# Kernel tuning notes

Hardware: AMD Instinct MI355X
Metric: run time of the kernel (lower is better)

Reference implementation:

```python
import jax, jax.numpy as jnp
import numpy as np

NUM_USERS = 100000
NUM_ITEMS = 50000
NUM_NODES = NUM_USERS + NUM_ITEMS
EMBED_DIM = 128
NUM_LAYERS = 3
CONTENT_DIM = 768
NUM_EDGES = 1000000
BATCH = 4096
LAMBDA_CONTENT = 0.1
INIT_STD = 0.1


def setup_inputs() -> dict:
    key = jax.random.key(0)
    ks = jax.random.split(key, 9)
    edge_index = jax.random.randint(ks[0], (2, NUM_EDGES), 0, NUM_NODES, dtype=jnp.int64 if jax.config.jax_enable_x64 else jnp.int32)
    edge_weight = jax.random.uniform(ks[1], (NUM_EDGES,), dtype=jnp.float32)
    batch_users = jax.random.randint(ks[2], (BATCH,), 0, NUM_USERS)
    batch_pos_items = jax.random.randint(ks[3], (BATCH,), 0, NUM_ITEMS)
    batch_neg_items = jax.random.randint(ks[4], (BATCH,), 0, NUM_ITEMS)
    item_content = jax.random.normal(ks[5], (NUM_ITEMS, CONTENT_DIM), dtype=jnp.float32)
    user_emb_w = INIT_STD * jax.random.normal(ks[6], (NUM_USERS, EMBED_DIM), dtype=jnp.float32)
    item_emb_w = INIT_STD * jax.random.normal(ks[7], (NUM_ITEMS, EMBED_DIM), dtype=jnp.float32)
    # nn.Linear(item_content_dim, embed_dim, bias=False): weight [embed_dim, content_dim]
    bound = 1.0 / np.sqrt(CONTENT_DIM)
    content_proj_w = jax.random.uniform(ks[8], (EMBED_DIM, CONTENT_DIM), minval=-bound, maxval=bound, dtype=jnp.float32)
    return {
        'edge_index': edge_index, 'edge_weight': edge_weight,
        'batch_users': batch_users, 'batch_pos_items': batch_pos_items,
        'batch_neg_items': batch_neg_items, 'item_content': item_content,
        'user_emb_w': user_emb_w, 'item_emb_w': item_emb_w,
        'content_proj_w': content_proj_w,
    }


def _lgconv(x, src, dst, ew, num_nodes):
    # PyG LGConv: gcn_norm(add_self_loops=False) then scatter-add at target.
    deg = jax.ops.segment_sum(ew, dst, num_segments=num_nodes)          # [N]
    dinv = jnp.where(deg > 0, jax.lax.rsqrt(deg), 0.0)
    norm = dinv[src] * ew * dinv[dst]                                    # [E]
    return jax.ops.segment_sum(norm[:, None] * x[src], dst, num_segments=num_nodes)


def _propagate(user_emb_w, item_emb_w, src, dst, ew):
    x = jnp.concatenate([user_emb_w, item_emb_w], axis=0)               # [N, D]
    acc = x
    for _ in range(NUM_LAYERS):
        x = _lgconv(x, src, dst, ew, NUM_NODES)
        acc = acc + x
    x_final = acc / (NUM_LAYERS + 1)
    return x_final[:NUM_USERS], x_final[NUM_USERS:]


def reference(edge_index, edge_weight, batch_users, batch_pos_items,
              batch_neg_items, item_content, user_emb_w, item_emb_w,
              content_proj_w):
    src, dst = edge_index[0], edge_index[1]
    u_final, i_final = _propagate(user_emb_w, item_emb_w, src, dst, edge_weight)
    u = u_final[batch_users]
    i_pos = i_final[batch_pos_items]
    i_neg = i_final[batch_neg_items]
    pos_score = jnp.sum(u * i_pos, axis=-1)
    neg_score = jnp.sum(u * i_neg, axis=-1)
    bpr = jnp.mean(jax.nn.softplus(-(pos_score - neg_score)))
    reg = jnp.mean(jnp.sum(u**2, axis=1) + jnp.sum(i_pos**2, axis=1) + jnp.sum(i_neg**2, axis=1)) * 1e-4
    proj = item_content @ content_proj_w.T                              # [I, D]
    align = jnp.mean((i_final - proj) ** 2)
    loss = bpr + reg + LAMBDA_CONTENT * align
    return loss, u_final, i_final
```

## Files before the change

kernel.cpp:

```cpp
#include <hip/hip_runtime.h>
#include <math.h>

#define NU 100000
#define NI 50000
#define NN 150000
#define D 128
#define NE 1000000
#define CD 768
#define BATCH 4096
#define NGEMM 782
#define NK (CD / 64)
#define PREPB 2832
#define ARMB 944

typedef short bf16x8 __attribute__((ext_vector_type(8)));
typedef float f32x4 __attribute__((ext_vector_type(4)));

static inline size_t alignup(size_t x, size_t a) { return (x + a - 1) / a * a; }

__device__ inline unsigned short f2bf(float f) {
  unsigned int u = __builtin_bit_cast(unsigned int, f);
  unsigned int r = (u + 0x7fffu + ((u >> 16) & 1u)) >> 16;
  return (unsigned short)r;
}
__device__ inline unsigned int pack2bf(float lo, float hi) {
  return (unsigned int)f2bf(lo) | ((unsigned int)f2bf(hi) << 16);
}
__device__ inline float bflo(unsigned int p) {
  return __builtin_bit_cast(float, p << 16);
}
__device__ inline float bfhi(unsigned int p) {
  return __builtin_bit_cast(float, p & 0xffff0000u);
}

#define ACC8(P, W)                                                        \
  a[0] = fmaf(W, bflo(P.x), a[0]); a[1] = fmaf(W, bfhi(P.x), a[1]);       \
  a[2] = fmaf(W, bflo(P.y), a[2]); a[3] = fmaf(W, bfhi(P.y), a[3]);       \
  a[4] = fmaf(W, bflo(P.z), a[4]); a[5] = fmaf(W, bfhi(P.z), a[5]);       \
  a[6] = fmaf(W, bflo(P.w), a[6]); a[7] = fmaf(W, bfhi(P.w), a[7]);

__device__ __forceinline__ void gather_rows(
    const int* __restrict__ row_ptr, const uint2* __restrict__ cedge,
    const uint4* __restrict__ xin, int n, int sub, float* a) {
  int beg = row_ptr[n], end = row_ptr[n + 1];
  int j = beg;
  for (; j + 4 <= end; j += 4) {
    uint2 e0 = cedge[j], e1 = cedge[j + 1], e2 = cedge[j + 2], e3 = cedge[j + 3];
    uint4 p0 = xin[(size_t)e0.x * 16 + sub];
    uint4 p1 = xin[(size_t)e1.x * 16 + sub];
    uint4 p2 = xin[(size_t)e2.x * 16 + sub];
    uint4 p3 = xin[(size_t)e3.x * 16 + sub];
    float w0 = __builtin_bit_cast(float, e0.y);
    float w1 = __builtin_bit_cast(float, e1.y);
    float w2 = __builtin_bit_cast(float, e2.y);
    float w3 = __builtin_bit_cast(float, e3.y);
    ACC8(p0, w0) ACC8(p1, w1) ACC8(p2, w2) ACC8(p3, w3)
  }
  for (; j < end; ++j) {
    uint2 e0 = cedge[j];
    uint4 p0 = xin[(size_t)e0.x * 16 + sub];
    float w0 = __builtin_bit_cast(float, e0.y);
    ACC8(p0, w0)
  }
}

__global__ __launch_bounds__(512) void prep_kernel(
    const int* __restrict__ dst, int* __restrict__ cnt, int* __restrict__ cpos,
    const float* __restrict__ uemb, const float* __restrict__ iemb,
    unsigned int* __restrict__ x0b,
    const float* __restrict__ W, const float* __restrict__ content,
    uint4* __restrict__ proj) {
  __shared__ unsigned short Asm[64 * 64];
  __shared__ unsigned short Bsm[128 * 64];

  int bid = blockIdx.x;
  int tid = threadIdx.x;
  int arm = bid % 3, slot = bid / 3;

  if (arm == 0) {
    int i = slot * 512 + tid;
    for (; i < NE; i += ARMB * 512)
      cpos[i] = atomicAdd(&cnt[dst[i]], 1);
    return;
  }
  if (arm == 1) {
    const size_t XT = (size_t)NN * D / 8;
    size_t t = (size_t)slot * 512 + tid;
    for (; t < XT; t += (size_t)ARMB * 512) {
      size_t f = t * 8;
      const float* p = (f < (size_t)NU * D) ? (uemb + f) : (iemb + (f - (size_t)NU * D));
      float4 a = *(const float4*)p;
      float4 b = *(const float4*)(p + 4);
      uint4 o;
      o.x = pack2bf(a.x, a.y); o.y = pack2bf(a.z, a.w);
      o.z = pack2bf(b.x, b.y); o.w = pack2bf(b.z, b.w);
      *(uint4*)(x0b + t * 4) = o;
    }
    return;
  }
  if (slot >= NGEMM) return;

  int w = tid >> 6, lane = tid & 63;
  int i0 = slot * 64;
  int lrow = lane & 15, kq = lane >> 4;

  f32x4 acc[4];
#pragma unroll
  for (int rt = 0; rt < 4; ++rt) acc[rt] = (f32x4){0.f, 0.f, 0.f, 0.f};

  int sr = tid >> 3, c8 = tid & 7;
  int arow_g = (i0 + sr < NI) ? (i0 + sr) : (NI - 1);
  const float* aG = content + (size_t)arow_g * CD + c8 * 8;
  const float* bG0 = W + (size_t)sr * CD + c8 * 8;
  const float* bG1 = W + (size_t)(sr + 64) * CD + c8 * 8;
  int aoff = (c8 * 16) ^ ((sr & 7) << 4);

  {
    float4 a0 = *(const float4*)(aG);
    float4 a1 = *(const float4*)(aG + 4);
    float4 p0 = *(const float4*)(bG0);
    float4 p1 = *(const float4*)(bG0 + 4);
    float4 q0 = *(const float4*)(bG1);
    float4 q1 = *(const float4*)(bG1 + 4);
    uint4 oa, ob, oc;
    oa.x = pack2bf(a0.x, a0.y); oa.y = pack2bf(a0.z, a0.w);
    oa.z = pack2bf(a1.x, a1.y); oa.w = pack2bf(a1.z, a1.w);
    ob.x = pack2bf(p0.x, p0.y); ob.y = pack2bf(p0.z, p0.w);
    ob.z = pack2bf(p1.x, p1.y); ob.w = pack2bf(p1.z, p1.w);
    oc.x = pack2bf(q0.x, q0.y); oc.y = pack2bf(q0.z, q0.w);
    oc.z = pack2bf(q1.x, q1.y); oc.w = pack2bf(q1.z, q1.w);
    *(uint4*)((char*)Asm + sr * 128 + aoff) = oa;
    *(uint4*)((char*)Bsm + sr * 128 + aoff) = ob;
    *(uint4*)((char*)Bsm + (sr + 64) * 128 + aoff) = oc;
  }
  __syncthreads();

  for (int kk = 0; kk < NK; ++kk) {
    bool more = kk < NK - 1;
    float4 a0, a1, p0, p1, q0, q1;
    if (more) {
      int k0 = (kk + 1) * 64;
      a0 = *(const float4*)(aG + k0);
      a1 = *(const float4*)(aG + k0 + 4);
      p0 = *(const float4*)(bG0 + k0);
      p1 = *(const float4*)(bG0 + k0 + 4);
      q0 = *(const float4*)(bG1 + k0);
      q1 = *(const float4*)(bG1 + k0 + 4);
    }
#pragma unroll
    for (int ks = 0; ks < 2; ++ks) {
      int kbyte = ks * 64 + kq * 16;
      bf16x8 af[4], bfr;
#pragma unroll
      for (int rt = 0; rt < 4; ++rt) {
        int row = rt * 16 + lrow;
        af[rt] = *(const bf16x8*)((char*)Asm + row * 128 + (kbyte ^ ((row & 7) << 4)));
      }
      {
        int row = w * 16 + lrow;
        bfr = *(const bf16x8*)((char*)Bsm + row * 128 + (kbyte ^ ((row & 7) << 4)));
      }
#pragma unroll
      for (int rt = 0; rt < 4; ++rt)
        acc[rt] = __builtin_amdgcn_mfma_f32_16x16x32_bf16(af[rt], bfr, acc[rt], 0, 0, 0);
    }
    __syncthreads();
    if (more) {
      uint4 oa, ob, oc;
      oa.x = pack2bf(a0.x, a0.y); oa.y = pack2bf(a0.z, a0.w);
      oa.z = pack2bf(a1.x, a1.y); oa.w = pack2bf(a1.z, a1.w);
      ob.x = pack2bf(p0.x, p0.y); ob.y = pack2bf(p0.z, p0.w);
      ob.z = pack2bf(p1.x, p1.y); ob.w = pack2bf(p1.z, p1.w);
      oc.x = pack2bf(q0.x, q0.y); oc.y = pack2bf(q0.z, q0.w);
      oc.z = pack2bf(q1.x, q1.y); oc.w = pack2bf(q1.z, q1.w);
      *(uint4*)((char*)Asm + sr * 128 + aoff) = oa;
      *(uint4*)((char*)Bsm + sr * 128 + aoff) = ob;
      *(uint4*)((char*)Bsm + (sr + 64) * 128 + aoff) = oc;
      __syncthreads();
    }
  }

  unsigned short* T = (unsigned short*)Bsm;
  int dcol = w * 16 + lrow;
#pragma unroll
  for (int rt = 0; rt < 4; ++rt)
#pragma unroll
    for (int j = 0; j < 4; ++j)
      T[(rt * 16 + kq * 4 + j) * 128 + dcol] = f2bf(acc[rt][j]);
  __syncthreads();
#pragma unroll
  for (int u0 = 0; u0 < 2; ++u0) {
    int u = u0 * 512 + tid;
    int r = u >> 4, s = u & 15;
    int it = i0 + r;
    if (it < NI) proj[(size_t)it * 16 + s] = ((const uint4*)T)[u];
  }
}


__global__ void scan_p1(const int* __restrict__ cnt, int* __restrict__ bsum) {
  __shared__ int s[256];
  int b = blockIdx.x;
  int i = b * 256 + threadIdx.x;
  s[threadIdx.x] = (i < NN) ? cnt[i] : 0;
  __syncthreads();
  for (int off = 128; off; off >>= 1) {
    if (threadIdx.x < off) s[threadIdx.x] += s[threadIdx.x + off];
    __syncthreads();
  }
  if (threadIdx.x == 0) bsum[b] = s[0];
}

__global__ __launch_bounds__(1024) void scan_p2(int* __restrict__ bsum, int nb) {
  __shared__ int s[1024];
  int t = threadIdx.x;
  int v = (t < nb) ? bsum[t] : 0;
  s[t] = v;
  __syncthreads();
  for (int off = 1; off < 1024; off <<= 1) {
    int u = (t >= off) ? s[t - off] : 0;
    __syncthreads();
    s[t] += u;
    __syncthreads();
  }
  if (t < nb) bsum[t] = s[t] - v;
}

__global__ void scan_p3(const int* __restrict__ cnt, const int* __restrict__ bsum,
                        int* __restrict__ row_ptr) {
  __shared__ int s[256];
  int b = blockIdx.x;
  int i = b * 256 + threadIdx.x;
  s[threadIdx.x] = (i < NN) ? cnt[i] : 0;
  __syncthreads();
  for (int off = 1; off < 256; off <<= 1) {
    int t = (threadIdx.x >= off) ? s[threadIdx.x - off] : 0;
    __syncthreads();
    s[threadIdx.x] += t;
    __syncthreads();
  }
  if (i < NN) row_ptr[i + 1] = bsum[b] + s[threadIdx.x];
  if (i == 0) row_ptr[0] = 0;
}

__global__ void fill_kernel(const int* __restrict__ src, const int* __restrict__ dst,
                            const float* __restrict__ ew, const int* __restrict__ row_ptr,
                            const int* __restrict__ cpos, uint2* __restrict__ cedge) {
  int i = blockIdx.x * blockDim.x + threadIdx.x;
  int stride = gridDim.x * blockDim.x;
  for (; i < NE; i += stride) {
    int p = row_ptr[dst[i]] + cpos[i];
    uint2 e;
    e.x = (unsigned int)src[i];
    e.y = __builtin_bit_cast(unsigned int, ew[i]);
    cedge[p] = e;
  }
}

__global__ void degrow_kernel(const int* __restrict__ row_ptr, const uint2* __restrict__ cedge,
                              float* __restrict__ dinv) {
  int n = blockIdx.x * blockDim.x + threadIdx.x;
  if (n >= NN) return;
  int beg = row_ptr[n], end = row_ptr[n + 1];
  float s = 0.f;
  for (int p = beg; p < end; ++p) s += __builtin_bit_cast(float, cedge[p].y);
  dinv[n] = (s > 0.f) ? rsqrtf(s) : 0.f;
}

__global__ void norm_kernel(uint2* __restrict__ cedge, const float* __restrict__ dinv) {
  int i = blockIdx.x * blockDim.x + threadIdx.x;
  int stride = gridDim.x * blockDim.x;
  for (; i < NE; i += stride) {
    uint2 e = cedge[i];
    float nm = dinv[e.x] * __builtin_bit_cast(float, e.y);
    cedge[i].y = __builtin_bit_cast(unsigned int, nm);
  }
}

__global__ __launch_bounds__(256) void gather_kernel(
    const int* __restrict__ row_ptr, const uint2* __restrict__ cedge,
    const float* __restrict__ dinv, const uint4* __restrict__ xin,
    uint4* __restrict__ yout) {
  int tid = threadIdx.x;
  int wv = tid >> 6, lane = tid & 63;
  int g = lane >> 4, sub = lane & 15;
  int n = blockIdx.x * 16 + wv * 4 + g;
  if (n >= NN) return;
  float a[8] = {0.f, 0.f, 0.f, 0.f, 0.f, 0.f, 0.f, 0.f};
  gather_rows(row_ptr, cedge, xin, n, sub, a);
  float sc = dinv[n];
  uint4 o;
  o.x = pack2bf(a[0] * sc, a[1] * sc);
  o.y = pack2bf(a[2] * sc, a[3] * sc);
  o.z = pack2bf(a[4] * sc, a[5] * sc);
  o.w = pack2bf(a[6] * sc, a[7] * sc);
  yout[(size_t)n * 16 + sub] = o;
}

__global__ __launch_bounds__(256) void final_kernel(
    const int* __restrict__ row_ptr, const uint2* __restrict__ cedge,
    const float* __restrict__ dinv, const uint4* __restrict__ x0b,
    const uint4* __restrict__ y1b, const uint4* __restrict__ y2b,
    const uint4* __restrict__ proj, float* __restrict__ OUT,
    float* __restrict__ partials) {
  __shared__ float wred[4];
  int tid = threadIdx.x;
  int wv = tid >> 6, lane = tid & 63;
  int g = lane >> 4, sub = lane & 15;
  int n = blockIdx.x * 16 + wv * 4 + g;
  if (n >= NN) return;
  float a[8] = {0.f, 0.f, 0.f, 0.f, 0.f, 0.f, 0.f, 0.f};
  gather_rows(row_ptr, cedge, y2b, n, sub, a);
  float sc = dinv[n];
  size_t r = (size_t)n * 16 + sub;
  uint4 q0 = x0b[r], q1 = y1b[r], q2 = y2b[r];
  float v[8];
  v[0] = (bflo(q0.x) + bflo(q1.x) + bflo(q2.x) + a[0] * sc) * 0.25f;
  v[1] = (bfhi(q0.x) + bfhi(q1.x) + bfhi(q2.x) + a[1] * sc) * 0.25f;
  v[2] = (bflo(q0.y) + bflo(q1.y) + bflo(q2.y) + a[2] * sc) * 0.25f;
  v[3] = (bfhi(q0.y) + bfhi(q1.y) + bfhi(q2.y) + a[3] * sc) * 0.25f;
  v[4] = (bflo(q0.z) + bflo(q1.z) + bflo(q2.z) + a[4] * sc) * 0.25f;
  v[5] = (bfhi(q0.z) + bfhi(q1.z) + bfhi(q2.z) + a[5] * sc) * 0.25f;
  v[6] = (bflo(q0.w) + bflo(q1.w) + bflo(q2.w) + a[6] * sc) * 0.25f;
  v[7] = (bfhi(q0.w) + bfhi(q1.w) + bfhi(q2.w) + a[7] * sc) * 0.25f;
  float* op = OUT + (size_t)n * D + sub * 8;
#pragma unroll
  for (int k = 0; k < 8; ++k) op[k] = v[k];

  if (blockIdx.x >= (NU / 16)) {
    uint4 pj = proj[(size_t)(n - NU) * 16 + sub];
    float d0 = v[0] - bflo(pj.x), d1 = v[1] - bfhi(pj.x);
    float d2 = v[2] - bflo(pj.y), d3 = v[3] - bfhi(pj.y);
    float d4 = v[4] - bflo(pj.z), d5 = v[5] - bfhi(pj.z);
    float d6 = v[6] - bflo(pj.w), d7 = v[7] - bfhi(pj.w);
    float m = d0 * d0 + d1 * d1 + d2 * d2 + d3 * d3 + d4 * d4 + d5 * d5 + d6 * d6 + d7 * d7;
    for (int off = 32; off; off >>= 1) m += __shfl_down(m, off);
    if (lane == 0) wred[wv] = m;
    __syncthreads();
    if (tid == 0)
      atomicAdd(&partials[blockIdx.x & 255], wred[0] + wred[1] + wred[2] + wred[3]);
  }
}

__global__ __launch_bounds__(256) void loss_batch(
    const int* __restrict__ bu, const int* __restrict__ bp, const int* __restrict__ bn,
    const float* __restrict__ OUT, float* __restrict__ accums) {
  __shared__ float wsp[4], wrg[4];
  int wv = threadIdx.x >> 6, lane = threadIdx.x & 63;
  int gw = blockIdx.x * 4 + wv;
  int nw = gridDim.x * 4;
  float lsp = 0.f, lrg = 0.f;
  for (int b = gw; b < BATCH; b += nw) {
    const float* u = OUT + (size_t)bu[b] * D;
    const float* ip = OUT + ((size_t)NU + bp[b]) * D;
    const float* in_ = OUT + ((size_t)NU + bn[b]) * D;
    float u0 = u[lane], u1 = u[lane + 64];
    float p0 = ip[lane], p1 = ip[lane + 64];
    float n0 = in_[lane], n1 = in_[lane + 64];
    float ps = u0 * p0 + u1 * p1;
    float ns = u0 * n0 + u1 * n1;
    float rg = u0 * u0 + u1 * u1 + p0 * p0 + p1 * p1 + n0 * n0 + n1 * n1;
    for (int off = 32; off; off >>= 1) {
      ps += __shfl_down(ps, off);
      ns += __shfl_down(ns, off);
      rg += __shfl_down(rg, off);
    }
    if (lane == 0) {
      float x = ns - ps;
      lsp += fmaxf(x, 0.f) + log1pf(expf(-fabsf(x)));
      lrg += rg;
    }
  }
  if (lane == 0) { wsp[wv] = lsp; wrg[wv] = lrg; }
  __syncthreads();
  if (threadIdx.x == 0) {
    atomicAdd(&accums[0], wsp[0] + wsp[1] + wsp[2] + wsp[3]);
    atomicAdd(&accums[1], wrg[0] + wrg[1] + wrg[2] + wrg[3]);
  }
}

__global__ void finalize_kernel(const float* __restrict__ accums,
                                const float* __restrict__ partials,
                                float* __restrict__ out0) {
  __shared__ float sm[4];
  int tid = threadIdx.x;
  float v = partials[tid];
  for (int off = 32; off; off >>= 1) v += __shfl_down(v, off);
  if ((tid & 63) == 0) sm[tid >> 6] = v;
  __syncthreads();
  if (tid == 0) {
    float align_sum = sm[0] + sm[1] + sm[2] + sm[3];
    float bpr = accums[0] / (float)BATCH;
    float reg = (accums[1] / (float)BATCH) * 1e-4f;
    float align = align_sum / (float)((size_t)NI * D);
    out0[0] = bpr + reg + 0.1f * align;
  }
}

extern "C" void kernel_launch(void* const* d_in, const int* in_sizes, int n_in,
                              void* d_out, int out_size, void* d_ws, size_t ws_size,
                              hipStream_t stream) {
  const int* edge_index = (const int*)d_in[0];
  const float* ew = (const float*)d_in[1];
  const int* bu = (const int*)d_in[2];
  const int* bp = (const int*)d_in[3];
  const int* bn = (const int*)d_in[4];
  const float* content = (const float*)d_in[5];
  const float* uemb = (const float*)d_in[6];
  const float* iemb = (const float*)d_in[7];
  const float* W = (const float*)d_in[8];
  const int* src = edge_index;
  const int* dst = edge_index + NE;
  float* outf = (float*)d_out;
  float* OUT = outf + 1;

  char* ws = (char*)d_ws;
  size_t off = 0;
  auto alloc = [&](size_t bytes) {
    void* p = ws + off;
    off = alignup(off + bytes, 256);
    return p;
  };
  unsigned int* x0b = (unsigned int*)alloc((size_t)NN * 64 * 4);
  unsigned int* y1b = (unsigned int*)alloc((size_t)NN * 64 * 4);
  unsigned int* y2b = (unsigned int*)alloc((size_t)NN * 64 * 4);
  uint4* proj = (uint4*)alloc((size_t)NI * 16 * 16);
  float* dinv = (float*)alloc((size_t)NN * 4);
  int* cnt = (int*)alloc((size_t)NN * 4);
  int* row_ptr = (int*)alloc((size_t)(NN + 1) * 4);
  int NB = (NN + 255) / 256;
  int* bsum = (int*)alloc((size_t)NB * 4);
  int* cpos = (int*)alloc((size_t)NE * 4);
  uint2* cedge = (uint2*)alloc((size_t)NE * 8);
  float* accums = (float*)alloc(16 + 256 * 4);
  float* partials = accums + 4;

  hipMemsetAsync(cnt, 0, (size_t)NN * 4, stream);
  hipMemsetAsync(accums, 0, 16 + 256 * 4, stream);

  prep_kernel<<<PREPB, 512, 0, stream>>>(dst, cnt, cpos, uemb, iemb, x0b, W, content, proj);
  scan_p1<<<NB, 256, 0, stream>>>(cnt, bsum);
  scan_p2<<<1, 1024, 0, stream>>>(bsum, NB);
  scan_p3<<<NB, 256, 0, stream>>>(cnt, bsum, row_ptr);
  fill_kernel<<<2048, 256, 0, stream>>>(src, dst, ew, row_ptr, cpos, cedge);
  degrow_kernel<<<NB, 256, 0, stream>>>(row_ptr, cedge, dinv);
  norm_kernel<<<2048, 256, 0, stream>>>(cedge, dinv);

  int LB = (NN + 15) / 16;
  gather_kernel<<<LB, 256, 0, stream>>>(row_ptr, cedge, dinv, (const uint4*)x0b, (uint4*)y1b);
  gather_kernel<<<LB, 256, 0, stream>>>(row_ptr, cedge, dinv, (const uint4*)y1b, (uint4*)y2b);
  final_kernel<<<LB, 256, 0, stream>>>(row_ptr, cedge, dinv,
                                       (const uint4*)x0b, (const uint4*)y1b, (const uint4*)y2b,
                                       proj, OUT, partials);

  loss_batch<<<64, 256, 0, stream>>>(bu, bp, bn, OUT, accums);
  finalize_kernel<<<1, 256, 0, stream>>>(accums, partials, outf);
}
```

Before: 332.2 us.

## Fold source-side degree norm into gather and rebalance prep kernel block roles

Removes the separate norm kernel that rewrote every edge weight with dinv[src], and instead multiplies by dinv[src] inside each gather loop. This saves one full read-modify-write pass over the edge array and a launch. The cost is an extra random 4-byte load per edge in each of the three propagation passes. The prep kernel also moves from an interleaved three-way split to fixed contiguous block counts: 128 blocks for atomic counting, 192 for bf16 conversion, and the rest for the GEMM.

```diff
diff --git a/kernel.cpp b/kernel.cpp
--- a/kernel.cpp
+++ b/kernel.cpp
@@ -10,8 +10,9 @@
 #define BATCH 4096
 #define NGEMM 782
 #define NK (CD / 64)
-#define PREPB 2832
-#define ARMB 944
+#define ABLK_AT 128
+#define ABLK_XC 192
+#define ARMTOT (ABLK_AT + ABLK_XC)
 
 typedef short bf16x8 __attribute__((ext_vector_type(8)));
 typedef float f32x4 __attribute__((ext_vector_type(4)));
@@ -41,7 +42,8 @@
 
 __device__ __forceinline__ void gather_rows(
     const int* __restrict__ row_ptr, const uint2* __restrict__ cedge,
-    const uint4* __restrict__ xin, int n, int sub, float* a) {
+    const float* __restrict__ dinv, const uint4* __restrict__ xin,
+    int n, int sub, float* a) {
   int beg = row_ptr[n], end = row_ptr[n + 1];
   int j = beg;
   for (; j + 4 <= end; j += 4) {
@@ -50,16 +52,16 @@
     uint4 p1 = xin[(size_t)e1.x * 16 + sub];
     uint4 p2 = xin[(size_t)e2.x * 16 + sub];
     uint4 p3 = xin[(size_t)e3.x * 16 + sub];
-    float w0 = __builtin_bit_cast(float, e0.y);
-    float w1 = __builtin_bit_cast(float, e1.y);
-    float w2 = __builtin_bit_cast(float, e2.y);
-    float w3 = __builtin_bit_cast(float, e3.y);
+    float w0 = dinv[e0.x] * __builtin_bit_cast(float, e0.y);
+    float w1 = dinv[e1.x] * __builtin_bit_cast(float, e1.y);
+    float w2 = dinv[e2.x] * __builtin_bit_cast(float, e2.y);
+    float w3 = dinv[e3.x] * __builtin_bit_cast(float, e3.y);
     ACC8(p0, w0) ACC8(p1, w1) ACC8(p2, w2) ACC8(p3, w3)
   }
   for (; j < end; ++j) {
     uint2 e0 = cedge[j];
     uint4 p0 = xin[(size_t)e0.x * 16 + sub];
-    float w0 = __builtin_bit_cast(float, e0.y);
+    float w0 = dinv[e0.x] * __builtin_bit_cast(float, e0.y);
     ACC8(p0, w0)
   }
 }
@@ -75,18 +77,18 @@
 
   int bid = blockIdx.x;
   int tid = threadIdx.x;
-  int arm = bid % 3, slot = bid / 3;
-
-  if (arm == 0) {
-    int i = slot * 512 + tid;
-    for (; i < NE; i += ARMB * 512)
+
+  if (bid < ABLK_AT) {
+    int i = bid * 512 + tid;
+    for (; i < NE; i += ABLK_AT * 512)
       cpos[i] = atomicAdd(&cnt[dst[i]], 1);
     return;
   }
-  if (arm == 1) {
+  if (bid < ARMTOT) {
+    int half = bid - ABLK_AT;
     const size_t XT = (size_t)NN * D / 8;
-    size_t t = (size_t)slot * 512 + tid;
-    for (; t < XT; t += (size_t)ARMB * 512) {
+    size_t t = (size_t)half * 512 + tid;
+    for (; t < XT; t += (size_t)ABLK_XC * 512) {
       size_t f = t * 8;
       const float* p = (f < (size_t)NU * D) ? (uemb + f) : (iemb + (f - (size_t)NU * D));
       float4 a = *(const float4*)p;
@@ -98,7 +100,7 @@
     }
     return;
   }
-  if (slot >= NGEMM) return;
+  int slot = bid - ARMTOT;
 
   int w = tid >> 6, lane = tid & 63;
   int i0 = slot * 64;
@@ -267,16 +269,6 @@
   dinv[n] = (s > 0.f) ? rsqrtf(s) : 0.f;
 }
 
-__global__ void norm_kernel(uint2* __restrict__ cedge, const float* __restrict__ dinv) {
-  int i = blockIdx.x * blockDim.x + threadIdx.x;
-  int stride = gridDim.x * blockDim.x;
-  for (; i < NE; i += stride) {
-    uint2 e = cedge[i];
-    float nm = dinv[e.x] * __builtin_bit_cast(float, e.y);
-    cedge[i].y = __builtin_bit_cast(unsigned int, nm);
-  }
-}
-
 __global__ __launch_bounds__(256) void gather_kernel(
     const int* __restrict__ row_ptr, const uint2* __restrict__ cedge,
     const float* __restrict__ dinv, const uint4* __restrict__ xin,
@@ -286,9 +278,9 @@
   int g = lane >> 4, sub = lane & 15;
   int n = blockIdx.x * 16 + wv * 4 + g;
   if (n >= NN) return;
+  float sc = dinv[n];
   float a[8] = {0.f, 0.f, 0.f, 0.f, 0.f, 0.f, 0.f, 0.f};
-  gather_rows(row_ptr, cedge, xin, n, sub, a);
-  float sc = dinv[n];
+  gather_rows(row_ptr, cedge, dinv, xin, n, sub, a);
   uint4 o;
   o.x = pack2bf(a[0] * sc, a[1] * sc);
   o.y = pack2bf(a[2] * sc, a[3] * sc);
@@ -309,11 +301,11 @@
   int g = lane >> 4, sub = lane & 15;
   int n = blockIdx.x * 16 + wv * 4 + g;
   if (n >= NN) return;
-  float a[8] = {0.f, 0.f, 0.f, 0.f, 0.f, 0.f, 0.f, 0.f};
-  gather_rows(row_ptr, cedge, y2b, n, sub, a);
-  float sc = dinv[n];
   size_t r = (size_t)n * 16 + sub;
   uint4 q0 = x0b[r], q1 = y1b[r], q2 = y2b[r];
+  float sc = dinv[n];
+  float a[8] = {0.f, 0.f, 0.f, 0.f, 0.f, 0.f, 0.f, 0.f};
+  gather_rows(row_ptr, cedge, dinv, y2b, n, sub, a);
   float v[8];
   v[0] = (bflo(q0.x) + bflo(q1.x) + bflo(q2.x) + a[0] * sc) * 0.25f;
   v[1] = (bfhi(q0.x) + bfhi(q1.x) + bfhi(q2.x) + a[1] * sc) * 0.25f;
@@ -438,13 +430,12 @@
   hipMemsetAsync(cnt, 0, (size_t)NN * 4, stream);
   hipMemsetAsync(accums, 0, 16 + 256 * 4, stream);
 
-  prep_kernel<<<PREPB, 512, 0, stream>>>(dst, cnt, cpos, uemb, iemb, x0b, W, content, proj);
+  prep_kernel<<<ARMTOT + NGEMM, 512, 0, stream>>>(dst, cnt, cpos, uemb, iemb, x0b, W, content, proj);
   scan_p1<<<NB, 256, 0, stream>>>(cnt, bsum);
   scan_p2<<<1, 1024, 0, stream>>>(bsum, NB);
   scan_p3<<<NB, 256, 0, stream>>>(cnt, bsum, row_ptr);
   fill_kernel<<<2048, 256, 0, stream>>>(src, dst, ew, row_ptr, cpos, cedge);
   degrow_kernel<<<NB, 256, 0, stream>>>(row_ptr, cedge, dinv);
-  norm_kernel<<<2048, 256, 0, stream>>>(cedge, dinv);
 
   int LB = (NN + 15) / 16;
   gather_kernel<<<LB, 256, 0, stream>>>(row_ptr, cedge, dinv, (const uint4*)x0b, (uint4*)y1b);
```

New measurement: 334.6 us. About the same (+0.7%).
